# Performance work log

Hardware: AMD Instinct MI355X
Metric: run time of the kernel (lower is better)

## Reference

```python
import jax, jax.numpy as jnp
import numpy as np

HEADS = 12
WINDOW = 128
EPS = 1e-5
MAX_WAVELENGTH = 10000.0
MASK_VALUE = -10000.0


def rms_norm(x, gamma):
    # keras LayerNormalization(rms_scaling=True): x * rsqrt(mean(x^2)+eps) * gamma
    return x * jax.lax.rsqrt(jnp.mean(jnp.square(x), axis=-1, keepdims=True) + EPS) * gamma


def rope(x):
    # x: [B, S, H, D]; keras_hub RotaryEmbedding (rotate-half, freqs tiled twice)
    S, D = x.shape[1], x.shape[-1]
    inv_freq = 1.0 / (MAX_WAVELENGTH ** (jnp.arange(0, D, 2, dtype=jnp.float32) / D))
    freqs = jnp.arange(S, dtype=jnp.float32)[:, None] * inv_freq[None, :]  # [S, D/2]
    emb = jnp.concatenate([freqs, freqs], axis=-1)  # [S, D]
    cos = jnp.cos(emb)[None, :, None, :]
    sin = jnp.sin(emb)[None, :, None, :]
    half = jnp.concatenate([-x[..., D // 2:], x[..., : D // 2]], axis=-1)
    return x * cos + half * sin


def setup_inputs() -> dict:
    key = jax.random.key(0)
    ks = jax.random.split(key, 8)
    B, S, Dm, Di = 2, 4096, 768, 1152
    return {
        "x": jax.random.normal(ks[0], (B, S, Dm), dtype=jnp.float32),
        "padding_mask": jnp.ones((B, S), dtype=jnp.int32),
        "w_qkv": jax.random.normal(ks[1], (Dm, 3 * Dm), dtype=jnp.float32) * 0.02,
        "w_o": jax.random.normal(ks[2], (Dm, Dm), dtype=jnp.float32) * 0.02,
        "gamma_attn": jnp.ones((Dm,), dtype=jnp.float32),
        "gamma_mlp": jnp.ones((Dm,), dtype=jnp.float32),
        "w_i0": jax.random.normal(ks[3], (Dm, Di), dtype=jnp.float32) * 0.02,
        "w_i1": jax.random.normal(ks[4], (Dm, Di), dtype=jnp.float32) * 0.02,
        "w_mo": jax.random.normal(ks[5], (Di, Dm), dtype=jnp.float32) * 0.02,
    }


def reference(x, padding_mask, w_qkv, w_o, gamma_attn, gamma_mlp, w_i0, w_i1, w_mo):
    B, S, Dm = x.shape
    H = HEADS
    Dh = Dm // H

    # --- attention block ---
    res = x
    h = rms_norm(x, gamma_attn)
    qkv = (h @ w_qkv).reshape(B, S, 3, H, Dh)
    q, k, v = qkv[:, :, 0], qkv[:, :, 1], qkv[:, :, 2]  # [B,S,H,Dh]
    q = rope(q)
    k = rope(k)
    scale = jnp.sqrt(jnp.asarray(Dh, dtype=x.dtype))
    scores = jnp.einsum("bqhd,bkhd->bhqk", q, k) / scale  # [B,H,S,S]

    idx = jnp.arange(S)
    sw_mask = (jnp.abs(idx[:, None] - idx[None, :]) <= WINDOW // 2).astype(x.dtype)
    scores = scores + (1.0 - sw_mask)[None, None, :, :] * MASK_VALUE
    p_mask = padding_mask.astype(x.dtype)[:, None, None, :]
    scores = scores + (1.0 - p_mask) * MASK_VALUE

    attn = jax.nn.softmax(scores.astype(jnp.float32), axis=-1).astype(x.dtype)
    out = jnp.einsum("bhqk,bkhd->bqhd", attn, v).reshape(B, S, Dm)
    x = res + out @ w_o

    # --- GeGLU MLP block ---
    res = x
    h = rms_norm(x, gamma_mlp)
    gate = jax.nn.gelu(h @ w_i0, approximate=True)
    x = res + (gate * (h @ w_i1)) @ w_mo
    return x
```

## Files before the change

kernel.cpp:

```cpp
#include <hip/hip_runtime.h>
#include <hip/hip_bf16.h>
#include <math.h>

#define SEQ   4096
#define BATCH 2
#define DM    768
#define DI    1152
#define NHEAD 12
#define DH    64
#define NTOK  (BATCH * SEQ)
#define HALFW 64

typedef unsigned short u16;
typedef __attribute__((ext_vector_type(8))) short   short8;
typedef __attribute__((ext_vector_type(4))) float   f32x4;
typedef __attribute__((ext_vector_type(8))) unsigned short ushort8;

__device__ __forceinline__ u16 f2bf(float f) {
    unsigned int u = __float_as_uint(f);
    u += 0x7fffu + ((u >> 16) & 1u);
    return (u16)(u >> 16);
}
__device__ __forceinline__ float bf2f(u16 b) {
    return __uint_as_float(((unsigned int)b) << 16);
}

__device__ __forceinline__ void gload16(const void* g, void* l) {
    __builtin_amdgcn_global_load_lds(
        (const __attribute__((address_space(1))) void*)g,
        (__attribute__((address_space(3))) void*)l, 16, 0, 0);
}

__device__ __forceinline__ float gelu_tanh(float v) {
    return 0.5f * v * (1.0f + tanhf(0.7978845608028654f * (v + 0.044715f * v * v * v)));
}

__global__ __launch_bounds__(256)
void wtrans_kernel(const float* __restrict__ W, u16* __restrict__ WT, int K, int N) {
    __shared__ float S[32][33];
    const int tn = blockIdx.x, tk = blockIdx.y;
    const int tx = threadIdx.x & 31, ty = threadIdx.x >> 5;
    #pragma unroll
    for (int i = 0; i < 4; ++i) {
        const int r = ty + i * 8;
        S[r][tx] = W[(size_t)(tk * 32 + r) * N + tn * 32 + tx];
    }
    __syncthreads();
    #pragma unroll
    for (int i = 0; i < 4; ++i) {
        const int r = ty + i * 8;
        WT[(size_t)(tn * 32 + r) * K + tk * 32 + tx] = f2bf(S[tx][r]);
    }
}

__global__ __launch_bounds__(256)
void rope_table_kernel(float* __restrict__ cosT, float* __restrict__ sinT) {
    const int id = blockIdx.x * 256 + threadIdx.x;
    const int j = id & 31, s = id >> 5;
    const float inv = powf(10000.0f, -(float)j * (1.0f / 32.0f));
    const float ph = (float)s * inv;
    cosT[id] = cosf(ph);
    sinT[id] = sinf(ph);
}

__global__ __launch_bounds__(256)
void rmsnorm_kernel(const float* __restrict__ x, const float* __restrict__ g,
                    u16* __restrict__ out) {
    const int row = blockIdx.x;
    const int t = threadIdx.x;
    const float* xr = x + (size_t)row * DM;
    float a = xr[t], b = xr[t + 256], c = xr[t + 512];
    float ss = a * a + b * b + c * c;
    #pragma unroll
    for (int o = 32; o > 0; o >>= 1) ss += __shfl_xor(ss, o);
    __shared__ float red[4];
    if ((t & 63) == 0) red[t >> 6] = ss;
    __syncthreads();
    float tot = red[0] + red[1] + red[2] + red[3];
    float inv = 1.0f / sqrtf(tot * (1.0f / DM) + 1e-5f);
    u16* orow = out + (size_t)row * DM;
    orow[t]       = f2bf(a * inv * g[t]);
    orow[t + 256] = f2bf(b * inv * g[t + 256]);
    orow[t + 512] = f2bf(c * inv * g[t + 512]);
}

template<int EPI, bool RES, bool OBF, bool DUAL>
__global__ __launch_bounds__(256)
void bgemm_kernel(const u16* __restrict__ A, const u16* __restrict__ B,
                  const u16* __restrict__ B2, void* __restrict__ Cv,
                  const float* __restrict__ R, int M, int N, int K, int nbn) {
    __shared__ u16 As[2 * 4096];
    __shared__ u16 Bs[2 * 4096];
    __shared__ u16 B2s[DUAL ? 2 * 4096 : 2];
    const int t = threadIdx.x;
    const int w = t >> 6, l = t & 63;
    const int wm = w >> 1, wn = w & 1;

    const int nb = gridDim.x;
    const int orig = blockIdx.x;
    const int qq = nb >> 3, rr = nb & 7;
    const int xcd = orig & 7, cidx = orig >> 3;
    const int wgid = (xcd < rr ? xcd * (qq + 1) : rr * (qq + 1) + (xcd - rr) * qq) + cidx;
    const int bm = wgid / nbn, bn = wgid % nbn;

    const int s0 = (w * 2 + 0) * 64 + l;
    const int s1 = (w * 2 + 1) * 64 + l;
    const int am0 = s0 >> 2, ak0 = ((s0 & 3) ^ ((s0 >> 3) & 3)) * 8;
    const int am1 = s1 >> 2, ak1 = ((s1 & 3) ^ ((s1 >> 3) & 3)) * 8;
    const u16* aSrc0 = A + (size_t)(bm * 128 + am0) * K + ak0;
    const u16* aSrc1 = A + (size_t)(bm * 128 + am1) * K + ak1;
    const u16* bSrc0 = B + (size_t)(bn * 128 + am0) * K + ak0;
    const u16* bSrc1 = B + (size_t)(bn * 128 + am1) * K + ak1;
    const u16* cSrc0 = DUAL ? B2 + (size_t)(bn * 128 + am0) * K + ak0 : nullptr;
    const u16* cSrc1 = DUAL ? B2 + (size_t)(bn * 128 + am1) * K + ak1 : nullptr;
    const int dS0 = (w * 2 + 0) * 512;
    const int dS1 = (w * 2 + 1) * 512;

    const int lm = l & 15, lk = l >> 4;
    const int xoff = ((lk ^ ((lm >> 1) & 3)) * 16);

    f32x4 acc[4][4] = {};
    f32x4 acc2[4][4] = {};

    const int nk = K >> 5;

#define STAGE(pp)  do {                                                        \
        u16* a_ = As + (pp) * 4096;  u16* b_ = Bs + (pp) * 4096;               \
        gload16(aSrc0, a_ + dS0);  gload16(aSrc1, a_ + dS1);                   \
        gload16(bSrc0, b_ + dS0);  gload16(bSrc1, b_ + dS1);                   \
        if (DUAL) { u16* c_ = B2s + (pp) * 4096;                               \
                    gload16(cSrc0, c_ + dS0);  gload16(cSrc1, c_ + dS1); }     \
        aSrc0 += 32; aSrc1 += 32; bSrc0 += 32; bSrc1 += 32;                    \
        if (DUAL) { cSrc0 += 32; cSrc1 += 32; }                                \
    } while (0)

    STAGE(0);
    __syncthreads();
    int p = 0;
    for (int kt = 0; kt < nk; ++kt) {
        if (kt + 1 < nk) STAGE(p ^ 1);

        const char* Abase = (const char*)As + p * 8192;
        const char* Bbase = (const char*)Bs + p * 8192;
        const char* Cbase = (const char*)B2s + p * 8192;
        short8 af[4], bfr[4], cfr[4];
        #pragma unroll
        for (int i = 0; i < 4; ++i) {
            af[i]  = *(const short8*)(Abase + (wm * 64 + i * 16 + lm) * 64 + xoff);
            bfr[i] = *(const short8*)(Bbase + (wn * 64 + i * 16 + lm) * 64 + xoff);
            if (DUAL) cfr[i] = *(const short8*)(Cbase + (wn * 64 + i * 16 + lm) * 64 + xoff);
        }
        #pragma unroll
        for (int i = 0; i < 4; ++i)
            #pragma unroll
            for (int j = 0; j < 4; ++j) {
                acc[i][j] = __builtin_amdgcn_mfma_f32_16x16x32_bf16(af[i], bfr[j], acc[i][j], 0, 0, 0);
                if (DUAL)
                    acc2[i][j] = __builtin_amdgcn_mfma_f32_16x16x32_bf16(af[i], cfr[j], acc2[i][j], 0, 0, 0);
            }
        __syncthreads();
        p ^= 1;
    }
#undef STAGE

    const int lg = l >> 4;
    float* Cf = (float*)Cv;
    u16*   Cb = (u16*)Cv;
    #pragma unroll
    for (int i = 0; i < 4; ++i) {
        const size_t row0 = (size_t)bm * 128 + wm * 64 + i * 16 + lg * 4;
        #pragma unroll
        for (int j = 0; j < 4; ++j) {
            const size_t col = (size_t)bn * 128 + wn * 64 + j * 16 + lm;
            #pragma unroll
            for (int r = 0; r < 4; ++r) {
                const size_t idx = (row0 + r) * (size_t)N + col;
                float v = acc[i][j][r];
                if (EPI == 3) v = gelu_tanh(v) * acc2[i][j][r];
                if (RES)      v += R[idx];
                if (OBF) Cb[idx] = f2bf(v);
                else     Cf[idx] = v;
            }
        }
    }
}

__device__ __forceinline__ u16* ldsAddr(u16* base, int row, int col) {
    const int ch = (col >> 3) ^ (row & 7);
    return base + row * 64 + ch * 8 + (col & 7);
}

__global__ __launch_bounds__(256)
void attn_kernel(const u16* __restrict__ qkv, const int* __restrict__ pmask,
                 const float* __restrict__ cosT, const float* __restrict__ sinT,
                 u16* __restrict__ out) {
    const int qt = blockIdx.x, h = blockIdx.y, b = blockIdx.z;
    const int q0 = qt * 64;
    const int t = threadIdx.x;
    const int w = t >> 6, l = t & 63;
    const int lm = l & 15, lg = l >> 4;

    __shared__ u16 Qs[64 * 64];
    __shared__ u16 Ks[64 * 64];
    __shared__ u16 Vt[64 * 64];
    __shared__ u16 Ps[64 * 64];

    {
        const int r = t >> 2, j0 = (t & 3) * 8;
        const int s = q0 + r;
        const u16* qrow = qkv + (size_t)(b * SEQ + s) * (3 * DM) + h * DH;
        ushort8 lo = *(const ushort8*)(qrow + j0);
        ushort8 hi = *(const ushort8*)(qrow + j0 + 32);
        const float* cr = cosT + (size_t)s * 32 + j0;
        const float* sr = sinT + (size_t)s * 32 + j0;
        ushort8 olo, ohi;
        #pragma unroll
        for (int e = 0; e < 8; ++e) {
            float c = cr[e], sn = sr[e];
            float xl = bf2f(lo[e]), xh = bf2f(hi[e]);
            olo[e] = f2bf(xl * c - xh * sn);
            ohi[e] = f2bf(xh * c + xl * sn);
        }
        *(ushort8*)ldsAddr(Qs, r, j0)      = olo;
        *(ushort8*)ldsAddr(Qs, r, j0 + 32) = ohi;
    }

    f32x4 oacc[4] = {};
    float Mrun[4], Lrun[4];
    #pragma unroll
    for (int r = 0; r < 4; ++r) { Mrun[r] = -3.0e38f; Lrun[r] = 0.f; }

    for (int kb = 0; kb < 3; ++kb) {
        const int kstart = q0 - 64 + kb * 64;
        __syncthreads();
        {
            const int r = t >> 2, j0 = (t & 3) * 8;
            const int kg = kstart + r;
            ushort8 olo = {}, ohi = {};
            if (kg >= 0 && kg < SEQ) {
                const u16* krow = qkv + (size_t)(b * SEQ + kg) * (3 * DM) + DM + h * DH;
                ushort8 lo = *(const ushort8*)(krow + j0);
                ushort8 hi = *(const ushort8*)(krow + j0 + 32);
                const float* cr = cosT + (size_t)kg * 32 + j0;
                const float* sr = sinT + (size_t)kg * 32 + j0;
                #pragma unroll
                for (int e = 0; e < 8; ++e) {
                    float c = cr[e], sn = sr[e];
                    float xl = bf2f(lo[e]), xh = bf2f(hi[e]);
                    olo[e] = f2bf(xl * c - xh * sn);
                    ohi[e] = f2bf(xh * c + xl * sn);
                }
            }
            *(ushort8*)ldsAddr(Ks, r, j0)      = olo;
            *(ushort8*)ldsAddr(Ks, r, j0 + 32) = ohi;
        }
        {
            const int key = l;
            const int kg = kstart + key;
            const int d0 = w * 16;
            if (kg >= 0 && kg < SEQ) {
                const u16* vrow = qkv + (size_t)(b * SEQ + kg) * (3 * DM) + 2 * DM + h * DH + d0;
                ushort8 v0 = *(const ushort8*)(vrow);
                ushort8 v1 = *(const ushort8*)(vrow + 8);
                #pragma unroll
                for (int e = 0; e < 8; ++e) {
                    *ldsAddr(Vt, d0 + e, key)     = v0[e];
                    *ldsAddr(Vt, d0 + 8 + e, key) = v1[e];
                }
            } else {
                #pragma unroll
                for (int e = 0; e < 16; ++e) *ldsAddr(Vt, d0 + e, key) = 0;
            }
        }
        __syncthreads();

        short8 af[2];
        #pragma unroll
        for (int ks = 0; ks < 2; ++ks)
            af[ks] = *(const short8*)ldsAddr(Qs, w * 16 + lm, ks * 32 + lg * 8);
        f32x4 sacc[4];
        #pragma unroll
        for (int j = 0; j < 4; ++j) {
            f32x4 z = {};
            #pragma unroll
            for (int ks = 0; ks < 2; ++ks) {
                short8 kf = *(const short8*)ldsAddr(Ks, j * 16 + lm, ks * 32 + lg * 8);
                z = __builtin_amdgcn_mfma_f32_16x16x32_bf16(af[ks], kf, z, 0, 0, 0);
            }
            sacc[j] = z;
        }

        float p[4][4];
        int pmj[4], kgj[4];
        #pragma unroll
        for (int j = 0; j < 4; ++j) {
            kgj[j] = kstart + j * 16 + lm;
            pmj[j] = (kgj[j] >= 0 && kgj[j] < SEQ) ? pmask[b * SEQ + kgj[j]] : 0;
        }
        float mt[4] = {-3.0e38f, -3.0e38f, -3.0e38f, -3.0e38f};
        #pragma unroll
        for (int j = 0; j < 4; ++j)
            #pragma unroll
            for (int r = 0; r < 4; ++r) {
                const int qg = q0 + w * 16 + lg * 4 + r;
                const int diff = qg - kgj[j];
                float v = sacc[j][r] * 0.125f;
                const bool valid = (pmj[j] != 0) && (diff <= HALFW) && (diff >= -HALFW);
                v = valid ? v : -3.0e38f;
                p[j][r] = v;
                mt[r] = fmaxf(mt[r], v);
            }

        #pragma unroll
        for (int r = 0; r < 4; ++r) {
            float m = mt[r];
            m = fmaxf(m, __shfl_xor(m, 1));
            m = fmaxf(m, __shfl_xor(m, 2));
            m = fmaxf(m, __shfl_xor(m, 4));
            m = fmaxf(m, __shfl_xor(m, 8));
            const float Mnew = fmaxf(Mrun[r], m);
            float ps = 0.f;
            #pragma unroll
            for (int j = 0; j < 4; ++j) {
                float e = (p[j][r] > -1.0e37f) ? expf(p[j][r] - Mnew) : 0.0f;
                p[j][r] = e; ps += e;
            }
            ps += __shfl_xor(ps, 1); ps += __shfl_xor(ps, 2);
            ps += __shfl_xor(ps, 4); ps += __shfl_xor(ps, 8);
            const float scale = expf(Mrun[r] - Mnew);
            Lrun[r] = Lrun[r] * scale + ps;
            Mrun[r] = Mnew;
            #pragma unroll
            for (int jd = 0; jd < 4; ++jd) oacc[jd][r] *= scale;
        }

        #pragma unroll
        for (int j = 0; j < 4; ++j)
            #pragma unroll
            for (int r = 0; r < 4; ++r)
                *ldsAddr(Ps, w * 16 + lg * 4 + r, j * 16 + lm) = f2bf(p[j][r]);

        #pragma unroll
        for (int ks = 0; ks < 2; ++ks) {
            short8 pa = *(const short8*)ldsAddr(Ps, w * 16 + lm, ks * 32 + lg * 8);
            #pragma unroll
            for (int jd = 0; jd < 4; ++jd) {
                short8 vb = *(const short8*)ldsAddr(Vt, jd * 16 + lm, ks * 32 + lg * 8);
                oacc[jd] = __builtin_amdgcn_mfma_f32_16x16x32_bf16(pa, vb, oacc[jd], 0, 0, 0);
            }
        }
    }

    #pragma unroll
    for (int r = 0; r < 4; ++r) {
        const float inv = (Lrun[r] > 0.f) ? 1.0f / Lrun[r] : 0.0f;
        const size_t row = (size_t)(b * SEQ + q0 + w * 16 + lg * 4 + r);
        #pragma unroll
        for (int jd = 0; jd < 4; ++jd)
            out[row * DM + h * DH + jd * 16 + lm] = f2bf(oacc[jd][r] * inv);
    }
}

extern "C" void kernel_launch(void* const* d_in, const int* in_sizes, int n_in,
                              void* d_out, int out_size, void* d_ws, size_t ws_size,
                              hipStream_t stream) {
    const float* x      = (const float*)d_in[0];
    const int*   pmask  = (const int*)  d_in[1];
    const float* w_qkv  = (const float*)d_in[2];
    const float* w_o    = (const float*)d_in[3];
    const float* g_attn = (const float*)d_in[4];
    const float* g_mlp  = (const float*)d_in[5];
    const float* w_i0   = (const float*)d_in[6];
    const float* w_i1   = (const float*)d_in[7];
    const float* w_mo   = (const float*)d_in[8];
    float* out = (float*)d_out;

    char* ws = (char*)d_ws;
    u16* Wqkv = (u16*)ws;                ws += (size_t)768 * 2304 * 2;
    u16* Wo   = (u16*)ws;                ws += (size_t)768 * 768 * 2;
    u16* Wi0  = (u16*)ws;                ws += (size_t)768 * 1152 * 2;
    u16* Wi1  = (u16*)ws;                ws += (size_t)768 * 1152 * 2;
    u16* Wmo  = (u16*)ws;                ws += (size_t)1152 * 768 * 2;
    u16* hB    = (u16*)ws;               ws += (size_t)NTOK * DM * 2;
    u16* qkvB  = (u16*)ws;               ws += (size_t)NTOK * 3 * DM * 2;
    u16* attnB = (u16*)ws;               ws += (size_t)NTOK * DM * 2;
    u16* prodB = (u16*)ws;               ws += (size_t)NTOK * DI * 2;
    float* ropeCos = (float*)ws;         ws += (size_t)SEQ * 32 * 4;
    float* ropeSin = (float*)ws;         ws += (size_t)SEQ * 32 * 4;

    rope_table_kernel<<<SEQ * 32 / 256, 256, 0, stream>>>(ropeCos, ropeSin);
    wtrans_kernel<<<dim3(2304 / 32, 768 / 32), 256, 0, stream>>>(w_qkv, Wqkv, 768, 2304);
    wtrans_kernel<<<dim3(768 / 32, 768 / 32),  256, 0, stream>>>(w_o,   Wo,   768, 768);
    wtrans_kernel<<<dim3(1152 / 32, 768 / 32), 256, 0, stream>>>(w_i0,  Wi0,  768, 1152);
    wtrans_kernel<<<dim3(1152 / 32, 768 / 32), 256, 0, stream>>>(w_i1,  Wi1,  768, 1152);
    wtrans_kernel<<<dim3(768 / 32, 1152 / 32), 256, 0, stream>>>(w_mo,  Wmo,  1152, 768);

    rmsnorm_kernel<<<NTOK, 256, 0, stream>>>(x, g_attn, hB);
    bgemm_kernel<0, false, true, false><<<(NTOK / 128) * (2304 / 128), 256, 0, stream>>>(
        hB, Wqkv, nullptr, qkvB, nullptr, NTOK, 2304, 768, 2304 / 128);
    attn_kernel<<<dim3(SEQ / 64, NHEAD, BATCH), 256, 0, stream>>>(
        qkvB, pmask, ropeCos, ropeSin, attnB);
    bgemm_kernel<0, true, false, false><<<(NTOK / 128) * (768 / 128), 256, 0, stream>>>(
        attnB, Wo, nullptr, out, x, NTOK, 768, 768, 768 / 128);
    rmsnorm_kernel<<<NTOK, 256, 0, stream>>>(out, g_mlp, hB);
    bgemm_kernel<3, false, true, true><<<(NTOK / 128) * (1152 / 128), 256, 0, stream>>>(
        hB, Wi0, Wi1, prodB, nullptr, NTOK, 1152, 768, 1152 / 128);
    bgemm_kernel<0, true, false, false><<<(NTOK / 128) * (768 / 128), 256, 0, stream>>>(
        prodB, Wmo, nullptr, out, out, NTOK, 768, 1152, 768 / 128);
}
```

Baseline: 332.3 us.

## Interleave GeGLU gate/up weights and compute both in one non-dual GEMM

The gate and up weight matrices are transposed into a single interleaved buffer, alternating 64-column blocks, so one ordinary 128-wide GEMM tile produces 64 gate and 64 up columns. The dual-B GEMM path with its second accumulator set and third LDS buffer is removed. The gate/up pairs are combined through an LDS exchange in the epilogue, where half the waves do the GELU-multiply and the store. This is meant to lower register and LDS pressure and raise occupancy, at the cost of twice as many blocks, an extra LDS round trip, and an idle half of the waves during the final store.

```diff
diff --git a/kernel.cpp b/kernel.cpp
--- a/kernel.cpp
+++ b/kernel.cpp
@@ -35,8 +35,10 @@
     return 0.5f * v * (1.0f + tanhf(0.7978845608028654f * (v + 0.044715f * v * v * v)));
 }
 
+template<bool ILV>
 __global__ __launch_bounds__(256)
-void wtrans_kernel(const float* __restrict__ W, u16* __restrict__ WT, int K, int N) {
+void wtrans_kernel(const float* __restrict__ W, u16* __restrict__ WT,
+                   int K, int N, int ofs) {
     __shared__ float S[32][33];
     const int tn = blockIdx.x, tk = blockIdx.y;
     const int tx = threadIdx.x & 31, ty = threadIdx.x >> 5;
@@ -49,7 +51,9 @@
     #pragma unroll
     for (int i = 0; i < 4; ++i) {
         const int r = ty + i * 8;
-        WT[(size_t)(tn * 32 + r) * K + tk * 32 + tx] = f2bf(S[tx][r]);
+        const int n = tn * 32 + r;
+        const int np = ILV ? ((n >> 6) * 128 + ofs + (n & 63)) : n;
+        WT[(size_t)np * K + tk * 32 + tx] = f2bf(S[tx][r]);
     }
 }
 
@@ -84,14 +88,14 @@
     orow[t + 512] = f2bf(c * inv * g[t + 512]);
 }
 
-template<int EPI, bool RES, bool OBF, bool DUAL>
+template<int EPI, bool RES, bool OBF>
 __global__ __launch_bounds__(256)
 void bgemm_kernel(const u16* __restrict__ A, const u16* __restrict__ B,
-                  const u16* __restrict__ B2, void* __restrict__ Cv,
-                  const float* __restrict__ R, int M, int N, int K, int nbn) {
-    __shared__ u16 As[2 * 4096];
-    __shared__ u16 Bs[2 * 4096];
-    __shared__ u16 B2s[DUAL ? 2 * 4096 : 2];
+                  void* __restrict__ Cv, const float* __restrict__ R,
+                  int M, int N, int K, int nbn) {
+    __shared__ u16 SM[16384];
+    u16* As = SM;
+    u16* Bs = SM + 8192;
     const int t = threadIdx.x;
     const int w = t >> 6, l = t & 63;
     const int wm = w >> 1, wn = w & 1;
@@ -111,8 +115,6 @@
     const u16* aSrc1 = A + (size_t)(bm * 128 + am1) * K + ak1;
     const u16* bSrc0 = B + (size_t)(bn * 128 + am0) * K + ak0;
     const u16* bSrc1 = B + (size_t)(bn * 128 + am1) * K + ak1;
-    const u16* cSrc0 = DUAL ? B2 + (size_t)(bn * 128 + am0) * K + ak0 : nullptr;
-    const u16* cSrc1 = DUAL ? B2 + (size_t)(bn * 128 + am1) * K + ak1 : nullptr;
     const int dS0 = (w * 2 + 0) * 512;
     const int dS1 = (w * 2 + 1) * 512;
 
@@ -120,7 +122,6 @@
     const int xoff = ((lk ^ ((lm >> 1) & 3)) * 16);
 
     f32x4 acc[4][4] = {};
-    f32x4 acc2[4][4] = {};
 
     const int nk = K >> 5;
 
@@ -128,10 +129,7 @@
         u16* a_ = As + (pp) * 4096;  u16* b_ = Bs + (pp) * 4096;               \
         gload16(aSrc0, a_ + dS0);  gload16(aSrc1, a_ + dS1);                   \
         gload16(bSrc0, b_ + dS0);  gload16(bSrc1, b_ + dS1);                   \
-        if (DUAL) { u16* c_ = B2s + (pp) * 4096;                               \
-                    gload16(cSrc0, c_ + dS0);  gload16(cSrc1, c_ + dS1); }     \
         aSrc0 += 32; aSrc1 += 32; bSrc0 += 32; bSrc1 += 32;                    \
-        if (DUAL) { cSrc0 += 32; cSrc1 += 32; }                                \
     } while (0)
 
     STAGE(0);
@@ -140,24 +138,19 @@
     for (int kt = 0; kt < nk; ++kt) {
         if (kt + 1 < nk) STAGE(p ^ 1);
 
-        const char* Abase = (const char*)As + p * 8192;
-        const char* Bbase = (const char*)Bs + p * 8192;
-        const char* Cbase = (const char*)B2s + p * 8192;
-        short8 af[4], bfr[4], cfr[4];
+        const char* Abase = (const char*)(As + p * 4096);
+        const char* Bbase = (const char*)(Bs + p * 4096);
+        short8 af[4], bfr[4];
         #pragma unroll
         for (int i = 0; i < 4; ++i) {
             af[i]  = *(const short8*)(Abase + (wm * 64 + i * 16 + lm) * 64 + xoff);
             bfr[i] = *(const short8*)(Bbase + (wn * 64 + i * 16 + lm) * 64 + xoff);
-            if (DUAL) cfr[i] = *(const short8*)(Cbase + (wn * 64 + i * 16 + lm) * 64 + xoff);
         }
         #pragma unroll
         for (int i = 0; i < 4; ++i)
             #pragma unroll
-            for (int j = 0; j < 4; ++j) {
+            for (int j = 0; j < 4; ++j)
                 acc[i][j] = __builtin_amdgcn_mfma_f32_16x16x32_bf16(af[i], bfr[j], acc[i][j], 0, 0, 0);
-                if (DUAL)
-                    acc2[i][j] = __builtin_amdgcn_mfma_f32_16x16x32_bf16(af[i], cfr[j], acc2[i][j], 0, 0, 0);
-            }
         __syncthreads();
         p ^= 1;
     }
@@ -166,6 +159,39 @@
     const int lg = l >> 4;
     float* Cf = (float*)Cv;
     u16*   Cb = (u16*)Cv;
+
+    if (EPI == 3) {
+        float* ex = (float*)SM;
+        if (wn == 1) {
+            #pragma unroll
+            for (int i = 0; i < 4; ++i)
+                #pragma unroll
+                for (int j = 0; j < 4; ++j)
+                    #pragma unroll
+                    for (int r = 0; r < 4; ++r)
+                        ex[(wm * 64 + i * 16 + lg * 4 + r) * 64 + j * 16 + lm] = acc[i][j][r];
+        }
+        __syncthreads();
+        if (wn == 0) {
+            #pragma unroll
+            for (int i = 0; i < 4; ++i) {
+                const int lrow0 = wm * 64 + i * 16 + lg * 4;
+                const size_t grow0 = (size_t)bm * 128 + lrow0;
+                #pragma unroll
+                for (int j = 0; j < 4; ++j) {
+                    const int c = j * 16 + lm;
+                    #pragma unroll
+                    for (int r = 0; r < 4; ++r) {
+                        const float up = ex[(lrow0 + r) * 64 + c];
+                        const float v = gelu_tanh(acc[i][j][r]) * up;
+                        Cb[(grow0 + r) * (size_t)N + (size_t)bn * 64 + c] = f2bf(v);
+                    }
+                }
+            }
+        }
+        return;
+    }
+
     #pragma unroll
     for (int i = 0; i < 4; ++i) {
         const size_t row0 = (size_t)bm * 128 + wm * 64 + i * 16 + lg * 4;
@@ -176,8 +202,7 @@
             for (int r = 0; r < 4; ++r) {
                 const size_t idx = (row0 + r) * (size_t)N + col;
                 float v = acc[i][j][r];
-                if (EPI == 3) v = gelu_tanh(v) * acc2[i][j][r];
-                if (RES)      v += R[idx];
+                if (RES) v += R[idx];
                 if (OBF) Cb[idx] = f2bf(v);
                 else     Cf[idx] = v;
             }
@@ -378,8 +403,7 @@
     char* ws = (char*)d_ws;
     u16* Wqkv = (u16*)ws;                ws += (size_t)768 * 2304 * 2;
     u16* Wo   = (u16*)ws;                ws += (size_t)768 * 768 * 2;
-    u16* Wi0  = (u16*)ws;                ws += (size_t)768 * 1152 * 2;
-    u16* Wi1  = (u16*)ws;                ws += (size_t)768 * 1152 * 2;
+    u16* Wmlp = (u16*)ws;                ws += (size_t)2304 * 768 * 2;
     u16* Wmo  = (u16*)ws;                ws += (size_t)1152 * 768 * 2;
     u16* hB    = (u16*)ws;               ws += (size_t)NTOK * DM * 2;
     u16* qkvB  = (u16*)ws;               ws += (size_t)NTOK * 3 * DM * 2;
@@ -389,22 +413,22 @@
     float* ropeSin = (float*)ws;         ws += (size_t)SEQ * 32 * 4;
 
     rope_table_kernel<<<SEQ * 32 / 256, 256, 0, stream>>>(ropeCos, ropeSin);
-    wtrans_kernel<<<dim3(2304 / 32, 768 / 32), 256, 0, stream>>>(w_qkv, Wqkv, 768, 2304);
-    wtrans_kernel<<<dim3(768 / 32, 768 / 32),  256, 0, stream>>>(w_o,   Wo,   768, 768);
-    wtrans_kernel<<<dim3(1152 / 32, 768 / 32), 256, 0, stream>>>(w_i0,  Wi0,  768, 1152);
-    wtrans_kernel<<<dim3(1152 / 32, 768 / 32), 256, 0, stream>>>(w_i1,  Wi1,  768, 1152);
-    wtrans_kernel<<<dim3(768 / 32, 1152 / 32), 256, 0, stream>>>(w_mo,  Wmo,  1152, 768);
+    wtrans_kernel<false><<<dim3(2304 / 32, 768 / 32), 256, 0, stream>>>(w_qkv, Wqkv, 768, 2304, 0);
+    wtrans_kernel<false><<<dim3(768 / 32, 768 / 32),  256, 0, stream>>>(w_o,   Wo,   768, 768, 0);
+    wtrans_kernel<true><<<dim3(1152 / 32, 768 / 32),  256, 0, stream>>>(w_i0,  Wmlp, 768, 1152, 0);
+    wtrans_kernel<true><<<dim3(1152 / 32, 768 / 32),  256, 0, stream>>>(w_i1,  Wmlp, 768, 1152, 64);
+    wtrans_kernel<false><<<dim3(768 / 32, 1152 / 32), 256, 0, stream>>>(w_mo,  Wmo,  1152, 768, 0);
 
     rmsnorm_kernel<<<NTOK, 256, 0, stream>>>(x, g_attn, hB);
-    bgemm_kernel<0, false, true, false><<<(NTOK / 128) * (2304 / 128), 256, 0, stream>>>(
-        hB, Wqkv, nullptr, qkvB, nullptr, NTOK, 2304, 768, 2304 / 128);
+    bgemm_kernel<0, false, true><<<(NTOK / 128) * (2304 / 128), 256, 0, stream>>>(
+        hB, Wqkv, qkvB, nullptr, NTOK, 2304, 768, 2304 / 128);
     attn_kernel<<<dim3(SEQ / 64, NHEAD, BATCH), 256, 0, stream>>>(
         qkvB, pmask, ropeCos, ropeSin, attnB);
-    bgemm_kernel<0, true, false, false><<<(NTOK / 128) * (768 / 128), 256, 0, stream>>>(
-        attnB, Wo, nullptr, out, x, NTOK, 768, 768, 768 / 128);
+    bgemm_kernel<0, true, false><<<(NTOK / 128) * (768 / 128), 256, 0, stream>>>(
+        attnB, Wo, out, x, NTOK, 768, 768, 768 / 128);
     rmsnorm_kernel<<<NTOK, 256, 0, stream>>>(out, g_mlp, hB);
-    bgemm_kernel<3, false, true, true><<<(NTOK / 128) * (1152 / 128), 256, 0, stream>>>(
-        hB, Wi0, Wi1, prodB, nullptr, NTOK, 1152, 768, 1152 / 128);
-    bgemm_kernel<0, true, false, false><<<(NTOK / 128) * (768 / 128), 256, 0, stream>>>(
-        prodB, Wmo, nullptr, out, out, NTOK, 768, 1152, 768 / 128);
-}
+    bgemm_kernel<3, false, true><<<(NTOK / 128) * (2304 / 128), 256, 0, stream>>>(
+        hB, Wmlp, prodB, nullptr, NTOK, 1152, 768, 2304 / 128);
+    bgemm_kernel<0, true, false><<<(NTOK / 128) * (768 / 128), 256, 0, stream>>>(
+        prodB, Wmo, out, out, NTOK, 768, 1152, 768 / 128);
+}
```

Result: faster. 298.1 us (-10.3%).
